# Performance work log

Measured on AMD Instinct MI355X. Metric: run time of the kernel, lower is better.

The kernel has to match this reference:

```python
import jax, jax.numpy as jnp
import numpy as np

D = 2048
G = 16


def setup_inputs() -> dict:
    key = jax.random.key(0)
    ks = jax.random.split(key, 7)
    scale = 1.0 / np.sqrt(D)
    x = jax.random.normal(ks[0], (4, 4096, D), dtype=jnp.float32)
    Wq = jax.random.uniform(ks[1], (D, D), jnp.float32, -scale, scale)
    bq = jax.random.uniform(ks[2], (D,), jnp.float32, -scale, scale)
    Wk = jax.random.uniform(ks[3], (D, D), jnp.float32, -scale, scale)
    bk = jax.random.uniform(ks[4], (D,), jnp.float32, -scale, scale)
    Wv = jax.random.uniform(ks[5], (D, D), jnp.float32, -scale, scale)
    bv = jax.random.uniform(ks[6], (D,), jnp.float32, -scale, scale)
    return {"x": x, "Wq": Wq, "bq": bq, "Wk": Wk, "bk": bk, "Wv": Wv, "bv": bv}


def reference(x, Wq, bq, Wk, bk, Wv, bv):
    B, T, Df = x.shape
    g = G
    d = Df // g  # per-group dim = 128
    q = x @ Wq.T + bq
    k = x @ Wk.T + bk
    v = x @ Wv.T + bv
    qs = q.reshape(B, T, g, d)
    ks_ = k.reshape(B, T, g, d)
    vs = v.reshape(B, T, g, d)
    # attention over the GROUP axis per token: scores are (B,T,g,g)
    scores = jnp.einsum('btgd,bthd->btgh', qs, ks_) / jnp.sqrt(jnp.asarray(d, x.dtype))
    att = jax.nn.softmax(scores, axis=-1)
    out = jnp.einsum('btgh,bthd->btgd', att, vs)
    return out.reshape(B, T, Df)
```

## Files before the change

### kernel.cpp

```cpp
#include <hip/hip_runtime.h>


#define DIM 2048
#define NTOT 6144
#define DG 128
#define NG 16
#define BK 32
#define KTILES (DIM / BK)

typedef __bf16 bf16x8 __attribute__((ext_vector_type(8)));
typedef float f32x4 __attribute__((ext_vector_type(4)));
typedef unsigned short u16;
typedef unsigned int u32;

__device__ __forceinline__ u16 f2bf(float f) {
  u32 u = __float_as_uint(f);
  u = (u + 0x7fffu + ((u >> 16) & 1u)) >> 16;
  return (u16)u;
}

__device__ __forceinline__ void gload16(const __bf16* g, __bf16* l) {
  __builtin_amdgcn_global_load_lds(
      (__attribute__((address_space(1))) void*)(void*)g,
      (__attribute__((address_space(3))) void*)l, 16, 0, 0);
}

__global__ __launch_bounds__(256) void cvt_kernel(const float* __restrict__ src,
                                                  u16* __restrict__ dst, int n4) {
  int i = blockIdx.x * 256 + threadIdx.x;
  if (i >= n4) return;
  float4 f = ((const float4*)src)[i];
  ushort4 o;
  o.x = f2bf(f.x); o.y = f2bf(f.y); o.z = f2bf(f.z); o.w = f2bf(f.w);
  ((ushort4*)dst)[i] = o;
}

__global__ __launch_bounds__(256) void cvtW_kernel(const float* __restrict__ wq,
                                                   const float* __restrict__ wk,
                                                   const float* __restrict__ wv,
                                                   u16* __restrict__ dst, int n4each) {
  int m = blockIdx.y;
  const float* s = (m == 0) ? wq : (m == 1) ? wk : wv;
  int i = blockIdx.x * 256 + threadIdx.x;
  if (i >= n4each) return;
  float4 f = ((const float4*)s)[i];
  ushort4 o;
  o.x = f2bf(f.x); o.y = f2bf(f.y); o.z = f2bf(f.z); o.w = f2bf(f.w);
  ((ushort4*)dst)[(size_t)m * n4each + i] = o;
}

__global__ __launch_bounds__(512, 1) void gemm_qkv(const __bf16* __restrict__ A,
                                                   const __bf16* __restrict__ W,
                                                   const float* __restrict__ bq,
                                                   const float* __restrict__ bk,
                                                   const float* __restrict__ bv,
                                                   u16* __restrict__ C) {
  __shared__ __bf16 lds[4 * 16384];

  const int tid = threadIdx.x;
  const int lane = tid & 63;
  const int w = tid >> 6;
  const int wm = w >> 2, wn = w & 3;
  const int lm = lane & 15, kq = lane >> 4;

  const int bid = blockIdx.x;
  const int swz = (bid & 7) * 192 + (bid >> 3);
  const int bm = swz % 64;
  const int bn = swz / 64;

  const __bf16* pA0 = A + (size_t)(bm * 256 + (tid >> 2)) * DIM + (tid & 3) * 8;
  const __bf16* pA1 = pA0 + (size_t)128 * DIM;
  const __bf16* pB0 = W + (size_t)(bn * 256 + (tid >> 2)) * DIM + (tid & 3) * 8;
  const __bf16* pB1 = pB0 + (size_t)128 * DIM;

#define STAGE(tt)                                                   \
  {                                                                 \
    __bf16* db = lds + ((tt) & 3) * 16384 + w * 512;                \
    gload16(pA0 + (tt) * BK, db);                                   \
    gload16(pA1 + (tt) * BK, db + 4096);                            \
    gload16(pB0 + (tt) * BK, db + 8192);                            \
    gload16(pB1 + (tt) * BK, db + 12288);                           \
  }

  f32x4 acc[8][4];
#pragma unroll
  for (int i = 0; i < 8; ++i)
#pragma unroll
    for (int j = 0; j < 4; ++j) acc[i][j] = (f32x4){0.f, 0.f, 0.f, 0.f};

  STAGE(0);
  STAGE(1);
  STAGE(2);

  for (int t = 0; t < KTILES; ++t) {
    if (t < KTILES - 2) {
      asm volatile("s_waitcnt vmcnt(8)" ::: "memory");
    } else if (t == KTILES - 2) {
      asm volatile("s_waitcnt vmcnt(4)" ::: "memory");
    } else {
      asm volatile("s_waitcnt vmcnt(0)" ::: "memory");
    }
    __builtin_amdgcn_s_barrier();
    asm volatile("" ::: "memory");
    __builtin_amdgcn_sched_barrier(0);

    if (t <= KTILES - 4) STAGE(t + 3);

    const __bf16* baseA = lds + (t & 3) * 16384 + (wm * 128 + lm) * BK + kq * 8;
    const __bf16* baseB = lds + (t & 3) * 16384 + 8192 + (wn * 64 + lm) * BK + kq * 8;
    bf16x8 af[8], bf[4];
#pragma unroll
    for (int i = 0; i < 8; ++i) af[i] = *(const bf16x8*)(baseA + i * 512);
#pragma unroll
    for (int j = 0; j < 4; ++j) bf[j] = *(const bf16x8*)(baseB + j * 512);

    __builtin_amdgcn_s_setprio(1);
#pragma unroll
    for (int i = 0; i < 8; ++i)
#pragma unroll
      for (int j = 0; j < 4; ++j)
        acc[i][j] = __builtin_amdgcn_mfma_f32_16x16x32_bf16(af[i], bf[j], acc[i][j], 0, 0, 0);
    __builtin_amdgcn_s_setprio(0);
  }
#undef STAGE

  const int mat = bn >> 3;
  const float* bias = (mat == 0) ? bq : (mat == 1) ? bk : bv;
  const int colb = bn * 256 + wn * 64 + lm;
  const int rowb = bm * 256 + wm * 128 + kq * 4;
#pragma unroll
  for (int i = 0; i < 8; ++i) {
#pragma unroll
    for (int j = 0; j < 4; ++j) {
      const int col = colb + j * 16;
      const float bs = bias[col & (DIM - 1)];
#pragma unroll
      for (int r = 0; r < 4; ++r) {
        const int row = rowb + i * 16 + r;
        C[(size_t)row * NTOT + col] = f2bf(acc[i][j][r] + bs);
      }
    }
  }
}

__device__ __forceinline__ void unpack8(uint4 v, float* f) {
  f[0] = __uint_as_float(v.x << 16);
  f[1] = __uint_as_float(v.x & 0xffff0000u);
  f[2] = __uint_as_float(v.y << 16);
  f[3] = __uint_as_float(v.y & 0xffff0000u);
  f[4] = __uint_as_float(v.z << 16);
  f[5] = __uint_as_float(v.z & 0xffff0000u);
  f[6] = __uint_as_float(v.w << 16);
  f[7] = __uint_as_float(v.w & 0xffff0000u);
}

__global__ __launch_bounds__(256) void attn_kernel(const u16* __restrict__ qkv,
                                                   float* __restrict__ out) {
  __shared__ __bf16 kv[4][4096];

  const int tid = threadIdx.x;
  const int lane = tid & 63;
  const int w = tid >> 6;
  const int token = blockIdx.x * 4 + w;
  const int g = lane & 15, s = lane >> 4;

  const __bf16* base = (const __bf16*)(qkv) + (size_t)token * NTOT;

  const __bf16* kvsrc = base + DIM;
#pragma unroll
  for (int i = 0; i < 8; ++i)
    gload16(kvsrc + i * 512 + lane * 8, (__bf16*)kv[w] + i * 512);

  float qf[32];
  const __bf16* qsrc = base + g * DG + s * 32;
#pragma unroll
  for (int j = 0; j < 4; ++j) {
    uint4 qc = *(const uint4*)(qsrc + j * 8);
    unpack8(qc, qf + j * 8);
  }

  asm volatile("s_waitcnt vmcnt(0)" ::: "memory");

  float sc[16];
  const __bf16* kl = (const __bf16*)kv[w] + s * 32;
#pragma unroll 4
  for (int h = 0; h < 16; ++h) {
    const uint4* kr = (const uint4*)(kl + h * DG);
    float a = 0.f;
#pragma unroll
    for (int j = 0; j < 4; ++j) {
      float kf[8];
      unpack8(kr[j], kf);
#pragma unroll
      for (int e = 0; e < 8; ++e) a = fmaf(qf[j * 8 + e], kf[e], a);
    }
    sc[h] = a;
  }
#pragma unroll
  for (int h = 0; h < 16; ++h) {
    float v = sc[h];
    v += __shfl_xor(v, 16);
    v += __shfl_xor(v, 32);
    sc[h] = v;
  }

  const float scale = 0.08838834764831845f;
  float mx = sc[0] * scale;
#pragma unroll
  for (int h = 1; h < 16; ++h) mx = fmaxf(mx, sc[h] * scale);
  float p[16], sum = 0.f;
#pragma unroll
  for (int h = 0; h < 16; ++h) {
    p[h] = __expf(sc[h] * scale - mx);
    sum += p[h];
  }
  const float inv = 1.f / sum;
#pragma unroll
  for (int h = 0; h < 16; ++h) p[h] *= inv;

  float o[32];
#pragma unroll
  for (int e = 0; e < 32; ++e) o[e] = 0.f;
  const __bf16* vl = (const __bf16*)kv[w] + 2048 + s * 32;
#pragma unroll 4
  for (int h = 0; h < 16; ++h) {
    const uint4* vr = (const uint4*)(vl + h * DG);
    const float ph = p[h];
#pragma unroll
    for (int j = 0; j < 4; ++j) {
      float vf[8];
      unpack8(vr[j], vf);
#pragma unroll
      for (int e = 0; e < 8; ++e) o[j * 8 + e] = fmaf(ph, vf[e], o[j * 8 + e]);
    }
  }

  float* ob = out + (size_t)token * DIM + g * DG + s * 32;
#pragma unroll
  for (int j = 0; j < 8; ++j) {
    float4 v4 = {o[j * 4], o[j * 4 + 1], o[j * 4 + 2], o[j * 4 + 3]};
    ((float4*)ob)[j] = v4;
  }
}

extern "C" void kernel_launch(void* const* d_in, const int* in_sizes, int n_in,
                              void* d_out, int out_size, void* d_ws, size_t ws_size,
                              hipStream_t stream) {
  const float* x  = (const float*)d_in[0];
  const float* Wq = (const float*)d_in[1];
  const float* bq = (const float*)d_in[2];
  const float* Wk = (const float*)d_in[3];
  const float* bk = (const float*)d_in[4];
  const float* Wv = (const float*)d_in[5];
  const float* bv = (const float*)d_in[6];
  float* out = (float*)d_out;

  const int M = in_sizes[0] / DIM;

  u16* xb  = (u16*)d_ws;
  u16* wb  = xb + (size_t)M * DIM;
  u16* qkv = wb + (size_t)3 * DIM * DIM;

  const int n4x = (M * DIM) / 4;
  cvt_kernel<<<dim3((n4x + 255) / 256), 256, 0, stream>>>(x, xb, n4x);
  const int n4w = (DIM * DIM) / 4;
  cvtW_kernel<<<dim3((n4w + 255) / 256, 3), 256, 0, stream>>>(Wq, Wk, Wv, wb, n4w);

  gemm_qkv<<<dim3((M / 256) * (NTOT / 256)), 512, 0, stream>>>(
      (const __bf16*)xb, (const __bf16*)wb, bq, bk, bv, qkv);

  attn_kernel<<<dim3(M / 4), 256, 0, stream>>>(qkv, out);
}
```

Baseline: 725.8 us.

## Restructure QKV GEMM mainloop into BK=64 double-buffered four-phase pipeline with swizzled LDS

The GEMM K-tile grows from 32 to 64 and the LDS ring drops from four stages to two. Each K-tile's MFMA work is split into four quadrant phases, and each phase also issues part of the next tile's global-to-LDS loads, with explicit barriers around it. LDS columns are XOR-swizzled so that fragment reads avoid bank conflicts. The aim is to overlap loads with MFMA more finely and cut barrier count per FLOP, at the cost of more barriers per tile and a shallower prefetch distance.

Result: no change. 719.7 us (-0.8%).

```diff
diff --git a/kernel.cpp b/kernel.cpp
--- a/kernel.cpp
+++ b/kernel.cpp
@@ -5,8 +5,8 @@
 #define NTOT 6144
 #define DG 128
 #define NG 16
-#define BK 32
-#define KTILES (DIM / BK)
+#define BK 64
+#define KT64 (DIM / BK)
 
 typedef __bf16 bf16x8 __attribute__((ext_vector_type(8)));
 typedef float f32x4 __attribute__((ext_vector_type(4)));
@@ -55,7 +55,7 @@
                                                    const float* __restrict__ bk,
                                                    const float* __restrict__ bv,
                                                    u16* __restrict__ C) {
-  __shared__ __bf16 lds[4 * 16384];
+  __shared__ __bf16 lds[2 * 32768];
 
   const int tid = threadIdx.x;
   const int lane = tid & 63;
@@ -68,18 +68,19 @@
   const int bm = swz % 64;
   const int bn = swz / 64;
 
-  const __bf16* pA0 = A + (size_t)(bm * 256 + (tid >> 2)) * DIM + (tid & 3) * 8;
-  const __bf16* pA1 = pA0 + (size_t)128 * DIM;
-  const __bf16* pB0 = W + (size_t)(bn * 256 + (tid >> 2)) * DIM + (tid & 3) * 8;
-  const __bf16* pB1 = pB0 + (size_t)128 * DIM;
-
-#define STAGE(tt)                                                   \
-  {                                                                 \
-    __bf16* db = lds + ((tt) & 3) * 16384 + w * 512;                \
-    gload16(pA0 + (tt) * BK, db);                                   \
-    gload16(pA1 + (tt) * BK, db + 4096);                            \
-    gload16(pB0 + (tt) * BK, db + 8192);                            \
-    gload16(pB1 + (tt) * BK, db + 12288);                           \
+  const int srow = tid >> 3;
+  const int scol = ((tid & 7) ^ ((tid >> 3) & 7)) * 8;
+  const __bf16* pA = A + (size_t)(bm * 256 + srow) * DIM + scol;
+  const __bf16* pB = W + (size_t)(bn * 256 + srow) * DIM + scol;
+
+#define STAGEH(tt, p)                                                         \
+  {                                                                           \
+    __bf16* db = lds + ((tt) & 1) * 32768 + ((p) >> 1) * 16384 +              \
+                 ((p) & 1) * 8192 + tid * 8;                                  \
+    const __bf16* sp = (((p) >> 1) == 0 ? pA : pB) +                          \
+                       (size_t)(((p) & 1) * 128) * DIM + (size_t)(tt) * BK;   \
+    gload16(sp, db);                                                          \
+    gload16(sp + (size_t)64 * DIM, db + 4096);                                \
   }
 
   f32x4 acc[8][4];
@@ -88,41 +89,66 @@
 #pragma unroll
     for (int j = 0; j < 4; ++j) acc[i][j] = (f32x4){0.f, 0.f, 0.f, 0.f};
 
-  STAGE(0);
-  STAGE(1);
-  STAGE(2);
-
-  for (int t = 0; t < KTILES; ++t) {
-    if (t < KTILES - 2) {
-      asm volatile("s_waitcnt vmcnt(8)" ::: "memory");
-    } else if (t == KTILES - 2) {
-      asm volatile("s_waitcnt vmcnt(4)" ::: "memory");
-    } else {
-      asm volatile("s_waitcnt vmcnt(0)" ::: "memory");
-    }
-    __builtin_amdgcn_s_barrier();
-    asm volatile("" ::: "memory");
-    __builtin_amdgcn_sched_barrier(0);
-
-    if (t <= KTILES - 4) STAGE(t + 3);
-
-    const __bf16* baseA = lds + (t & 3) * 16384 + (wm * 128 + lm) * BK + kq * 8;
-    const __bf16* baseB = lds + (t & 3) * 16384 + 8192 + (wn * 64 + lm) * BK + kq * 8;
-    bf16x8 af[8], bf[4];
-#pragma unroll
-    for (int i = 0; i < 8; ++i) af[i] = *(const bf16x8*)(baseA + i * 512);
-#pragma unroll
-    for (int j = 0; j < 4; ++j) bf[j] = *(const bf16x8*)(baseB + j * 512);
-
-    __builtin_amdgcn_s_setprio(1);
-#pragma unroll
-    for (int i = 0; i < 8; ++i)
-#pragma unroll
-      for (int j = 0; j < 4; ++j)
-        acc[i][j] = __builtin_amdgcn_mfma_f32_16x16x32_bf16(af[i], bf[j], acc[i][j], 0, 0, 0);
-    __builtin_amdgcn_s_setprio(0);
-  }
-#undef STAGE
+  int aoff[2][2], boff[2][2];
+#pragma unroll
+  for (int ih = 0; ih < 2; ++ih)
+#pragma unroll
+    for (int kk = 0; kk < 2; ++kk)
+      aoff[ih][kk] = (wm * 128 + ih * 64 + lm) * 64 + (((kk << 2) | kq) ^ (lm & 7)) * 8;
+#pragma unroll
+  for (int jh = 0; jh < 2; ++jh)
+#pragma unroll
+    for (int kk = 0; kk < 2; ++kk)
+      boff[jh][kk] = (wn * 64 + jh * 32 + lm) * 64 + (((kk << 2) | kq) ^ (lm & 7)) * 8;
+
+  bf16x8 af[4][2], bfr[2][2];
+
+#define PH(tv, ih, jh, dostage, p)                                            \
+  {                                                                           \
+    const __bf16* bufb = lds + ((tv) & 1) * 32768;                            \
+    if ((jh) == 0) {                                                          \
+      _Pragma("unroll") for (int ir = 0; ir < 4; ++ir)                        \
+        _Pragma("unroll") for (int kk = 0; kk < 2; ++kk)                      \
+          af[ir][kk] = *(const bf16x8*)(bufb + aoff[ih][kk] + ir * 1024);     \
+    }                                                                         \
+    _Pragma("unroll") for (int jr = 0; jr < 2; ++jr)                          \
+      _Pragma("unroll") for (int kk = 0; kk < 2; ++kk)                        \
+        bfr[jr][kk] = *(const bf16x8*)(bufb + 16384 + boff[jh][kk] + jr * 1024); \
+    if (dostage) STAGEH((tv) + 1, p);                                         \
+    __builtin_amdgcn_sched_barrier(0);                                       \
+    asm volatile("s_barrier" ::: "memory");                                   \
+    asm volatile("s_waitcnt lgkmcnt(0)" ::: "memory");                        \
+    __builtin_amdgcn_sched_barrier(0);                                       \
+    __builtin_amdgcn_s_setprio(1);                                            \
+    _Pragma("unroll") for (int ir = 0; ir < 4; ++ir)                          \
+      _Pragma("unroll") for (int jr = 0; jr < 2; ++jr)                        \
+        _Pragma("unroll") for (int kk = 0; kk < 2; ++kk)                      \
+          acc[(ih) * 4 + ir][(jh) * 2 + jr] =                                 \
+              __builtin_amdgcn_mfma_f32_16x16x32_bf16(                        \
+                  af[ir][kk], bfr[jr][kk], acc[(ih) * 4 + ir][(jh) * 2 + jr], \
+                  0, 0, 0);                                                   \
+    __builtin_amdgcn_s_setprio(0);                                            \
+    if ((p) == 3) asm volatile("s_waitcnt vmcnt(0)" ::: "memory");            \
+    asm volatile("s_barrier" ::: "memory");                                   \
+  }
+
+  STAGEH(0, 0) STAGEH(0, 1) STAGEH(0, 2) STAGEH(0, 3)
+  asm volatile("s_waitcnt vmcnt(0)" ::: "memory");
+  asm volatile("s_barrier" ::: "memory");
+
+#pragma unroll 1
+  for (int t = 0; t < KT64 - 1; ++t) {
+    PH(t, 0, 0, 1, 0)
+    PH(t, 0, 1, 1, 1)
+    PH(t, 1, 0, 1, 2)
+    PH(t, 1, 1, 1, 3)
+  }
+  PH(KT64 - 1, 0, 0, 0, 0)
+  PH(KT64 - 1, 0, 1, 0, 1)
+  PH(KT64 - 1, 1, 0, 0, 2)
+  PH(KT64 - 1, 1, 1, 0, 3)
+#undef PH
+#undef STAGEH
 
   const int mat = bn >> 3;
   const float* bias = (mat == 0) ? bq : (mat == 1) ? bk : bv;
```
